# Optimization experiments

Measured on AMD Instinct MI355X. Metric: run time of the kernel, lower is better.

The kernel has to match this reference:

```python
import jax, jax.numpy as jnp
import numpy as np

B, T, D, H, W = 128, 1024, 8, 64, 128  # batch, time points, data_size, hidden_size, width_size


def setup_inputs() -> dict:
    key = jax.random.key(0)
    ks = jax.random.split(key, 18)
    nrm = lambda k, shp, s: jax.random.normal(k, shp, dtype=jnp.float32) * s
    inp = {
        'ts': jnp.arange(T, dtype=jnp.float32),
        # cubic spline coefficients per interval: value(t) = d*s^3 + c*s^2 + b*s + a, s = t - ts[i]
        'coeff_d': nrm(ks[0], (B, T - 1, D), 0.02),
        'coeff_c': nrm(ks[1], (B, T - 1, D), 0.05),
        'coeff_b': nrm(ks[2], (B, T - 1, D), 0.1),
        'coeff_a': nrm(ks[3], (B, T - 1, D), 1.0),
        # initial MLP: data -> width -> width -> hidden (relu hidden, identity final)
        'iw0': nrm(ks[4], (W, D), 1.0 / np.sqrt(D)), 'ib0': jnp.zeros((W,), jnp.float32),
        'iw1': nrm(ks[5], (W, W), 1.0 / np.sqrt(W)), 'ib1': jnp.zeros((W,), jnp.float32),
        'iw2': nrm(ks[6], (H, W), 1.0 / np.sqrt(W)), 'ib2': jnp.zeros((H,), jnp.float32),
        # vector-field MLP: hidden -> width -> width -> hidden*data (softplus hidden, tanh final)
        'fw0': nrm(ks[7], (W, H), 1.0 / np.sqrt(H)), 'fb0': jnp.zeros((W,), jnp.float32),
        'fw1': nrm(ks[8], (W, W), 1.0 / np.sqrt(W)), 'fb1': jnp.zeros((W,), jnp.float32),
        'fw2': nrm(ks[9], (H * D, W), 1.0 / np.sqrt(W)), 'fb2': jnp.zeros((H * D,), jnp.float32),
        # readout hidden -> 1
        'lw': nrm(ks[10], (1, H), 1.0 / np.sqrt(H)), 'lb': jnp.zeros((1,), jnp.float32),
    }
    return inp


def _init_mlp(x, iw0, ib0, iw1, ib1, iw2, ib2):
    h = jax.nn.relu(x @ iw0.T + ib0)
    h = jax.nn.relu(h @ iw1.T + ib1)
    return h @ iw2.T + ib2


def _vector_field(y, fw0, fb0, fw1, fb1, fw2, fb2, Hn, Dn):
    h = jax.nn.softplus(y @ fw0.T + fb0)
    h = jax.nn.softplus(h @ fw1.T + fb1)
    h = jnp.tanh(h @ fw2.T + fb2)
    return h.reshape(y.shape[0], Hn, Dn)  # f(y): [B, H, D]


def _forward(ts, coeff_d, coeff_c, coeff_b, coeff_a,
             iw0, ib0, iw1, ib1, iw2, ib2,
             fw0, fb0, fw1, fb1, fw2, fb2, lw, lb):
    Bn, Tm1, Dn = coeff_a.shape
    Hn = iw2.shape[0]
    # control.evaluate(ts[0]) == a of the first interval (local time s=0)
    y0 = _init_mlp(coeff_a[:, 0, :], iw0, ib0, iw1, ib1, iw2, ib2)  # [B, H]
    hs = jnp.diff(ts)  # [T-1] step sizes
    dT = jnp.transpose(coeff_d, (1, 0, 2))  # [T-1, B, D]
    cT = jnp.transpose(coeff_c, (1, 0, 2))
    bT = jnp.transpose(coeff_b, (1, 0, 2))

    def ode_rhs(s, y, d, c, b):
        # dX/dt = 3 d s^2 + 2 c s + b (derivative of the cubic spline)
        dX = (3.0 * d * s + 2.0 * c) * s + b  # [B, D]
        F = _vector_field(y, fw0, fb0, fw1, fb1, fw2, fb2, Hn, Dn)
        return jnp.einsum('bhd,bd->bh', F, dX)

    @jax.checkpoint
    def step(y, x):
        d, c, b, h = x
        k1 = ode_rhs(0.0, y, d, c, b)
        k2 = ode_rhs(0.5 * h, y + 0.5 * h * k1, d, c, b)
        k3 = ode_rhs(0.5 * h, y + 0.5 * h * k2, d, c, b)
        k4 = ode_rhs(h, y + h * k3, d, c, b)
        return y + (h / 6.0) * (k1 + 2.0 * k2 + 2.0 * k3 + k4), None

    yT, _ = jax.lax.scan(step, y0, (dT, cT, bT, hs))
    return jax.nn.sigmoid(yT @ lw.T + lb)[:, 0]  # [B]


def reference(ts, coeff_d, coeff_c, coeff_b, coeff_a,
              iw0, ib0, iw1, ib1, iw2, ib2,
              fw0, fb0, fw1, fb1, fw2, fb2, lw, lb):
    return _forward(ts, coeff_d, coeff_c, coeff_b, coeff_a,
                    iw0, ib0, iw1, ib1, iw2, ib2,
                    fw0, fb0, fw1, fb1, fw2, fb2, lw, lb)
```

## Files before the change

### kernel.cpp

```cpp
#include <hip/hip_runtime.h>
#include <math.h>

#define PAD(i) ((i) + (((i) >> 5) << 2))

__device__ __forceinline__ float softplus_f(float x) {
    return fmaxf(x, 0.f) + __logf(1.f + __expf(-fabsf(x)));
}
__device__ __forceinline__ float tanh_f(float x) {
    float ax = fabsf(x);
    float e  = __expf(-2.f * ax);
    float r  = (1.f - e) * __builtin_amdgcn_rcpf(1.f + e);
    return copysignf(r, x);
}

__global__ __launch_bounds__(512, 1)
void ncde_kernel(const float* __restrict__ ts,
                 const float* __restrict__ cd,
                 const float* __restrict__ cc,
                 const float* __restrict__ cb,
                 const float* __restrict__ ca,
                 const float* __restrict__ iw0, const float* __restrict__ ib0,
                 const float* __restrict__ iw1, const float* __restrict__ ib1,
                 const float* __restrict__ iw2, const float* __restrict__ ib2,
                 const float* __restrict__ fw0, const float* __restrict__ fb0,
                 const float* __restrict__ fw1, const float* __restrict__ fb1,
                 const float* __restrict__ fw2, const float* __restrict__ fb2,
                 const float* __restrict__ lw, const float* __restrict__ lb,
                 float* __restrict__ out, int T)
{
    const int b   = blockIdx.x;
    const int t   = threadIdx.x;
    const int w4  = t >> 2;
    const int j4  = t & 3;
    const int dd  = t & 7;
    const int hh  = t >> 3;
    const int Tm1 = T - 1;

    __shared__ __align__(16) float ytmp[68];
    __shared__ __align__(16) float h1s[140];
    __shared__ __align__(16) float h2s[140];
    __shared__ __align__(16) float dcb[24];
    __shared__ float xin[8];
    __shared__ float hs_s[1024];

    for (int i = t; i < Tm1; i += 512) hs_s[i] = ts[i + 1] - ts[i];

    float w0r[16], w1r[32], w2r[128];
    {
        const float4* p0 = (const float4*)(fw0 + (size_t)w4 * 64 + j4 * 16);
        #pragma unroll
        for (int q = 0; q < 4; ++q) ((float4*)w0r)[q] = p0[q];
        const float4* p1 = (const float4*)(fw1 + (size_t)w4 * 128 + j4 * 32);
        #pragma unroll
        for (int q = 0; q < 8; ++q) ((float4*)w1r)[q] = p1[q];
        const float4* p2 = (const float4*)(fw2 + (size_t)t * 128);
        #pragma unroll
        for (int q = 0; q < 32; ++q) ((float4*)w2r)[q] = p2[q];
    }
    const float fb0r = fb0[w4];
    const float fb1r = fb1[w4];
    const float fb2r = fb2[t];

    if (t < 8) xin[t] = ca[((size_t)b * Tm1) * 8 + t];
    __syncthreads();

    if (t < 128) {
        float a = ib0[t];
        #pragma unroll
        for (int k = 0; k < 8; ++k) a += iw0[t * 8 + k] * xin[k];
        h1s[PAD(t)] = fmaxf(a, 0.f);
    }
    __syncthreads();

    {
        const float* wrow = iw1 + (size_t)w4 * 128 + j4 * 32;
        const int base = j4 * 36;
        float a = 0.f;
        #pragma unroll
        for (int k = 0; k < 32; ++k) a += wrow[k] * h1s[base + k];
        a += __shfl_xor(a, 1); a += __shfl_xor(a, 2);
        if (j4 == 0) h2s[PAD(w4)] = fmaxf(a + ib1[w4], 0.f);
    }
    __syncthreads();

    if (t < 256) {
        const float* wrow = iw2 + (size_t)w4 * 128 + j4 * 32;
        const int base = j4 * 36;
        float a = 0.f;
        #pragma unroll
        for (int k = 0; k < 32; ++k) a += wrow[k] * h2s[base + k];
        a += __shfl_xor(a, 1); a += __shfl_xor(a, 2);
        if (j4 == 0) ytmp[PAD(w4)] = a + ib2[w4];
    }
    __syncthreads();

    float yy_r   = ytmp[PAD(hh)];
    float ksum_r = 0.f;

    const int b0 = j4 * 16 + ((j4 >> 1) << 2);
    const int b1 = j4 * 36;

    float4 dcbv = {0.f, 0.f, 0.f, 0.f};
    if (t < 6) {
        const float* p = (t < 2) ? cd : ((t < 4) ? cc : cb);
        dcbv = ((const float4*)(p + ((size_t)b * Tm1) * 8))[t & 1];
    }

    for (int i = 0; i < Tm1; ++i) {
        const float hstep = hs_s[i];

        #pragma unroll
        for (int st = 0; st < 4; ++st) {
            const float s = (st == 0) ? 0.f : ((st == 3) ? hstep : 0.5f * hstep);

            {
                float a0 = 0.f, a1 = 0.f;
                #pragma unroll
                for (int q = 0; q < 4; ++q) {
                    float4 y4 = ((const float4*)(ytmp + b0))[q];
                    a0 += w0r[4 * q]     * y4.x;
                    a1 += w0r[4 * q + 1] * y4.y;
                    a0 += w0r[4 * q + 2] * y4.z;
                    a1 += w0r[4 * q + 3] * y4.w;
                }
                float a = a0 + a1;
                a += __shfl_xor(a, 1); a += __shfl_xor(a, 2);
                if (j4 == 0) h1s[PAD(w4)] = softplus_f(a + fb0r);
            }
            __syncthreads();

            if (st == 0 && t < 6) {
                ((float4*)dcb)[t] = dcbv;
                const size_t nbase =
                    ((size_t)b * Tm1 + ((i + 1 < Tm1) ? (i + 1) : 0)) * 8;
                const float* p = (t < 2) ? cd : ((t < 4) ? cc : cb);
                dcbv = ((const float4*)(p + nbase))[t & 1];
            }

            {
                float a0 = 0.f, a1 = 0.f, a2 = 0.f, a3 = 0.f;
                #pragma unroll
                for (int q = 0; q < 8; ++q) {
                    float4 h4 = ((const float4*)(h1s + b1))[q];
                    a0 += w1r[4 * q]     * h4.x;
                    a1 += w1r[4 * q + 1] * h4.y;
                    a2 += w1r[4 * q + 2] * h4.z;
                    a3 += w1r[4 * q + 3] * h4.w;
                }
                float a = (a0 + a1) + (a2 + a3);
                a += __shfl_xor(a, 1); a += __shfl_xor(a, 2);
                if (j4 == 0) h2s[PAD(w4)] = softplus_f(a + fb1r);
            }
            __syncthreads();

            {
                float a0 = 0.f, a1 = 0.f, a2 = 0.f, a3 = 0.f;
                #pragma unroll
                for (int q = 0; q < 32; ++q) {
                    float4 h4 = *(const float4*)&h2s[4 * q + ((q >> 3) << 2)];
                    a0 += w2r[4 * q]     * h4.x;
                    a1 += w2r[4 * q + 1] * h4.y;
                    a2 += w2r[4 * q + 2] * h4.z;
                    a3 += w2r[4 * q + 3] * h4.w;
                }
                float g = tanh_f(((a0 + a1) + (a2 + a3)) + fb2r);
                float dX = (3.f * dcb[dd] * s + 2.f * dcb[8 + dd]) * s + dcb[16 + dd];
                float pr = g * dX;
                pr += __shfl_xor(pr, 1); pr += __shfl_xor(pr, 2); pr += __shfl_xor(pr, 4);
                float ynext;
                if (st == 0)      { ksum_r  = pr;        ynext = yy_r + 0.5f * hstep * pr; }
                else if (st == 1) { ksum_r += 2.f * pr;  ynext = yy_r + 0.5f * hstep * pr; }
                else if (st == 2) { ksum_r += 2.f * pr;  ynext = yy_r + hstep * pr; }
                else              { yy_r += (hstep * (1.f / 6.f)) * (ksum_r + pr); ynext = yy_r; }
                if (dd == 0) ytmp[PAD(hh)] = ynext;
            }
            __syncthreads();
        }
    }

    if (t < 64) {
        float v = ytmp[PAD(t)] * lw[t];
        #pragma unroll
        for (int off = 1; off < 64; off <<= 1) v += __shfl_xor(v, off);
        if (t == 0) out[b] = 1.f / (1.f + __expf(-(v + lb[0])));
    }
}

extern "C" void kernel_launch(void* const* d_in, const int* in_sizes, int n_in,
                              void* d_out, int out_size, void* d_ws, size_t ws_size,
                              hipStream_t stream) {
    const float* ts  = (const float*)d_in[0];
    const float* cd  = (const float*)d_in[1];
    const float* cc  = (const float*)d_in[2];
    const float* cb  = (const float*)d_in[3];
    const float* ca  = (const float*)d_in[4];
    const float* iw0 = (const float*)d_in[5];
    const float* ib0 = (const float*)d_in[6];
    const float* iw1 = (const float*)d_in[7];
    const float* ib1 = (const float*)d_in[8];
    const float* iw2 = (const float*)d_in[9];
    const float* ib2 = (const float*)d_in[10];
    const float* fw0 = (const float*)d_in[11];
    const float* fb0 = (const float*)d_in[12];
    const float* fw1 = (const float*)d_in[13];
    const float* fb1 = (const float*)d_in[14];
    const float* fw2 = (const float*)d_in[15];
    const float* fb2 = (const float*)d_in[16];
    const float* lw  = (const float*)d_in[17];
    const float* lb  = (const float*)d_in[18];
    float* out = (float*)d_out;

    const int T = in_sizes[0];
    const int B = out_size;

    ncde_kernel<<<B, 512, 0, stream>>>(ts, cd, cc, cb, ca,
                                       iw0, ib0, iw1, ib1, iw2, ib2,
                                       fw0, fb0, fw1, fb1, fw2, fb2,
                                       lw, lb, out, T);
}
```

Before: 5.945 ms.

## Double block to 1024 threads, halving per-thread dot-product work in vector-field MLP

Each batch element's block grows from 512 to 1024 threads, so every matvec layer is split across twice as many lanes (8 lanes per hidden unit, 2 lanes per output), with extra shuffle reductions. The sequential RK4 chain is latency bound, so shorter per-thread FMA chains should shorten each stage. Spline coefficients are now loaded per-thread into registers instead of being staged through shared memory. The cost is more shuffle steps, barriers that now span 16 waves, and a fixed 128 blocks that occupy only 128 CUs.

```diff
diff --git a/kernel.cpp b/kernel.cpp
--- a/kernel.cpp
+++ b/kernel.cpp
@@ -13,7 +13,7 @@
     return copysignf(r, x);
 }
 
-__global__ __launch_bounds__(512, 1)
+__global__ __launch_bounds__(1024, 1)
 void ncde_kernel(const float* __restrict__ ts,
                  const float* __restrict__ cd,
                  const float* __restrict__ cc,
@@ -30,84 +30,89 @@
 {
     const int b   = blockIdx.x;
     const int t   = threadIdx.x;
-    const int w4  = t >> 2;
-    const int j4  = t & 3;
-    const int dd  = t & 7;
-    const int hh  = t >> 3;
+    const int w8  = t >> 3;
+    const int j8  = t & 7;
+    const int o2  = t >> 1;
+    const int j2  = t & 1;
+    const int dd2 = (t >> 1) & 7;
+    const int hh  = t >> 4;
     const int Tm1 = T - 1;
 
     __shared__ __align__(16) float ytmp[68];
     __shared__ __align__(16) float h1s[140];
     __shared__ __align__(16) float h2s[140];
-    __shared__ __align__(16) float dcb[24];
-    __shared__ float xin[8];
     __shared__ float hs_s[1024];
 
-    for (int i = t; i < Tm1; i += 512) hs_s[i] = ts[i + 1] - ts[i];
-
-    float w0r[16], w1r[32], w2r[128];
-    {
-        const float4* p0 = (const float4*)(fw0 + (size_t)w4 * 64 + j4 * 16);
-        #pragma unroll
-        for (int q = 0; q < 4; ++q) ((float4*)w0r)[q] = p0[q];
-        const float4* p1 = (const float4*)(fw1 + (size_t)w4 * 128 + j4 * 32);
-        #pragma unroll
-        for (int q = 0; q < 8; ++q) ((float4*)w1r)[q] = p1[q];
-        const float4* p2 = (const float4*)(fw2 + (size_t)t * 128);
-        #pragma unroll
-        for (int q = 0; q < 32; ++q) ((float4*)w2r)[q] = p2[q];
-    }
-    const float fb0r = fb0[w4];
-    const float fb1r = fb1[w4];
-    const float fb2r = fb2[t];
-
-    if (t < 8) xin[t] = ca[((size_t)b * Tm1) * 8 + t];
+    for (int i = t; i < Tm1; i += 1024) hs_s[i] = ts[i + 1] - ts[i];
+
+    float w0r[8], w1r[16], w2r[64];
+    {
+        const float4* p0 = (const float4*)(fw0 + (size_t)w8 * 64 + j8 * 8);
+        ((float4*)w0r)[0] = p0[0];
+        ((float4*)w0r)[1] = p0[1];
+        const float4* p1 = (const float4*)(fw1 + (size_t)w8 * 128 + j8 * 16);
+        #pragma unroll
+        for (int q = 0; q < 4; ++q) ((float4*)w1r)[q] = p1[q];
+        const float4* p2 = (const float4*)(fw2 + (size_t)o2 * 128 + j2 * 64);
+        #pragma unroll
+        for (int q = 0; q < 16; ++q) ((float4*)w2r)[q] = p2[q];
+    }
+    const float fb0r = fb0[w8];
+    const float fb1r = fb1[w8];
+    const float fb2r = fb2[o2];
+
+    {
+        float a = iw0[w8 * 8 + j8] * ca[((size_t)b * Tm1) * 8 + j8];
+        a += __shfl_xor(a, 1); a += __shfl_xor(a, 2); a += __shfl_xor(a, 4);
+        if (j8 == 0) h1s[PAD(w8)] = fmaxf(a + ib0[w8], 0.f);
+    }
     __syncthreads();
-
-    if (t < 128) {
-        float a = ib0[t];
-        #pragma unroll
-        for (int k = 0; k < 8; ++k) a += iw0[t * 8 + k] * xin[k];
-        h1s[PAD(t)] = fmaxf(a, 0.f);
+    {
+        const int base = j8 * 16 + ((j8 >> 1) << 2);
+        const float4* wr = (const float4*)(iw1 + (size_t)w8 * 128 + j8 * 16);
+        float a = 0.f;
+        #pragma unroll
+        for (int q = 0; q < 4; ++q) {
+            float4 wv = wr[q];
+            float4 hv = *(const float4*)&h1s[base + 4 * q];
+            a += wv.x * hv.x + wv.y * hv.y + wv.z * hv.z + wv.w * hv.w;
+        }
+        a += __shfl_xor(a, 1); a += __shfl_xor(a, 2); a += __shfl_xor(a, 4);
+        if (j8 == 0) h2s[PAD(w8)] = fmaxf(a + ib1[w8], 0.f);
     }
     __syncthreads();
-
-    {
-        const float* wrow = iw1 + (size_t)w4 * 128 + j4 * 32;
-        const int base = j4 * 36;
+    {
+        const int j16 = t & 15;
+        const int base = j16 * 8 + ((j16 >> 2) << 2);
+        const float4* wr = (const float4*)(iw2 + (size_t)hh * 128 + j16 * 8);
         float a = 0.f;
         #pragma unroll
-        for (int k = 0; k < 32; ++k) a += wrow[k] * h1s[base + k];
+        for (int q = 0; q < 2; ++q) {
+            float4 wv = wr[q];
+            float4 hv = *(const float4*)&h2s[base + 4 * q];
+            a += wv.x * hv.x + wv.y * hv.y + wv.z * hv.z + wv.w * hv.w;
+        }
         a += __shfl_xor(a, 1); a += __shfl_xor(a, 2);
-        if (j4 == 0) h2s[PAD(w4)] = fmaxf(a + ib1[w4], 0.f);
-    }
-    __syncthreads();
-
-    if (t < 256) {
-        const float* wrow = iw2 + (size_t)w4 * 128 + j4 * 32;
-        const int base = j4 * 36;
-        float a = 0.f;
-        #pragma unroll
-        for (int k = 0; k < 32; ++k) a += wrow[k] * h2s[base + k];
-        a += __shfl_xor(a, 1); a += __shfl_xor(a, 2);
-        if (j4 == 0) ytmp[PAD(w4)] = a + ib2[w4];
+        a += __shfl_xor(a, 4); a += __shfl_xor(a, 8);
+        if ((t & 15) == 0) ytmp[PAD(hh)] = a + ib2[hh];
     }
     __syncthreads();
 
     float yy_r   = ytmp[PAD(hh)];
     float ksum_r = 0.f;
 
-    const int b0 = j4 * 16 + ((j4 >> 1) << 2);
-    const int b1 = j4 * 36;
-
-    float4 dcbv = {0.f, 0.f, 0.f, 0.f};
-    if (t < 6) {
-        const float* p = (t < 2) ? cd : ((t < 4) ? cc : cb);
-        dcbv = ((const float4*)(p + ((size_t)b * Tm1) * 8))[t & 1];
-    }
+    const int b0 = j8 * 8  + ((j8 >> 2) << 2);
+    const int b1 = j8 * 16 + ((j8 >> 1) << 2);
+    const int b2 = j2 * 72;
+
+    const float* pd = cd + ((size_t)b * Tm1) * 8 + dd2;
+    const float* pc = cc + ((size_t)b * Tm1) * 8 + dd2;
+    const float* pb = cb + ((size_t)b * Tm1) * 8 + dd2;
+    float dn = pd[0], cn = pc[0], bn = pb[0];
 
     for (int i = 0; i < Tm1; ++i) {
         const float hstep = hs_s[i];
+        const float d_r = dn, c_r = cn, b_r = bn;
 
         #pragma unroll
         for (int st = 0; st < 4; ++st) {
@@ -116,63 +121,62 @@
             {
                 float a0 = 0.f, a1 = 0.f;
                 #pragma unroll
-                for (int q = 0; q < 4; ++q) {
-                    float4 y4 = ((const float4*)(ytmp + b0))[q];
+                for (int q = 0; q < 2; ++q) {
+                    float4 y4 = *(const float4*)&ytmp[b0 + 4 * q];
                     a0 += w0r[4 * q]     * y4.x;
                     a1 += w0r[4 * q + 1] * y4.y;
                     a0 += w0r[4 * q + 2] * y4.z;
                     a1 += w0r[4 * q + 3] * y4.w;
                 }
                 float a = a0 + a1;
-                a += __shfl_xor(a, 1); a += __shfl_xor(a, 2);
-                if (j4 == 0) h1s[PAD(w4)] = softplus_f(a + fb0r);
+                a += __shfl_xor(a, 1); a += __shfl_xor(a, 2); a += __shfl_xor(a, 4);
+                if (j8 == 0) h1s[PAD(w8)] = softplus_f(a + fb0r);
             }
             __syncthreads();
 
-            if (st == 0 && t < 6) {
-                ((float4*)dcb)[t] = dcbv;
-                const size_t nbase =
-                    ((size_t)b * Tm1 + ((i + 1 < Tm1) ? (i + 1) : 0)) * 8;
-                const float* p = (t < 2) ? cd : ((t < 4) ? cc : cb);
-                dcbv = ((const float4*)(p + nbase))[t & 1];
+            if (st == 0) {
+                const int nidx = (i + 1 < Tm1) ? (i + 1) : 0;
+                dn = pd[nidx * 8]; cn = pc[nidx * 8]; bn = pb[nidx * 8];
             }
 
             {
                 float a0 = 0.f, a1 = 0.f, a2 = 0.f, a3 = 0.f;
                 #pragma unroll
-                for (int q = 0; q < 8; ++q) {
-                    float4 h4 = ((const float4*)(h1s + b1))[q];
+                for (int q = 0; q < 4; ++q) {
+                    float4 h4 = *(const float4*)&h1s[b1 + 4 * q];
                     a0 += w1r[4 * q]     * h4.x;
                     a1 += w1r[4 * q + 1] * h4.y;
                     a2 += w1r[4 * q + 2] * h4.z;
                     a3 += w1r[4 * q + 3] * h4.w;
                 }
                 float a = (a0 + a1) + (a2 + a3);
-                a += __shfl_xor(a, 1); a += __shfl_xor(a, 2);
-                if (j4 == 0) h2s[PAD(w4)] = softplus_f(a + fb1r);
+                a += __shfl_xor(a, 1); a += __shfl_xor(a, 2); a += __shfl_xor(a, 4);
+                if (j8 == 0) h2s[PAD(w8)] = softplus_f(a + fb1r);
             }
             __syncthreads();
 
             {
                 float a0 = 0.f, a1 = 0.f, a2 = 0.f, a3 = 0.f;
                 #pragma unroll
-                for (int q = 0; q < 32; ++q) {
-                    float4 h4 = *(const float4*)&h2s[4 * q + ((q >> 3) << 2)];
+                for (int q = 0; q < 16; ++q) {
+                    float4 h4 = *(const float4*)&h2s[b2 + 4 * q + ((q >> 3) << 2)];
                     a0 += w2r[4 * q]     * h4.x;
                     a1 += w2r[4 * q + 1] * h4.y;
                     a2 += w2r[4 * q + 2] * h4.z;
                     a3 += w2r[4 * q + 3] * h4.w;
                 }
-                float g = tanh_f(((a0 + a1) + (a2 + a3)) + fb2r);
-                float dX = (3.f * dcb[dd] * s + 2.f * dcb[8 + dd]) * s + dcb[16 + dd];
+                float a = (a0 + a1) + (a2 + a3);
+                a += __shfl_xor(a, 1);
+                float g = tanh_f(a + fb2r);
+                float dX = (3.f * d_r * s + 2.f * c_r) * s + b_r;
                 float pr = g * dX;
-                pr += __shfl_xor(pr, 1); pr += __shfl_xor(pr, 2); pr += __shfl_xor(pr, 4);
+                pr += __shfl_xor(pr, 2); pr += __shfl_xor(pr, 4); pr += __shfl_xor(pr, 8);
                 float ynext;
                 if (st == 0)      { ksum_r  = pr;        ynext = yy_r + 0.5f * hstep * pr; }
                 else if (st == 1) { ksum_r += 2.f * pr;  ynext = yy_r + 0.5f * hstep * pr; }
                 else if (st == 2) { ksum_r += 2.f * pr;  ynext = yy_r + hstep * pr; }
                 else              { yy_r += (hstep * (1.f / 6.f)) * (ksum_r + pr); ynext = yy_r; }
-                if (dd == 0) ytmp[PAD(hh)] = ynext;
+                if ((t & 15) == 0) ytmp[PAD(hh)] = ynext;
             }
             __syncthreads();
         }
@@ -213,8 +217,8 @@
     const int T = in_sizes[0];
     const int B = out_size;
 
-    ncde_kernel<<<B, 512, 0, stream>>>(ts, cd, cc, cb, ca,
-                                       iw0, ib0, iw1, ib1, iw2, ib2,
-                                       fw0, fb0, fw1, fb1, fw2, fb2,
-                                       lw, lb, out, T);
-}
+    ncde_kernel<<<B, 1024, 0, stream>>>(ts, cd, cc, cb, ca,
+                                        iw0, ib0, iw1, ib1, iw2, ib2,
+                                        fw0, fb0, fw1, fb1, fw2, fb2,
+                                        lw, lb, out, T);
+}
```

Measured after the change: 9.675 ms. 62.7% more time.
